# Performance work log

Measured on AMD Instinct MI355X. Metric: run time of the kernel, lower is better.

Reference implementation:

```python
import jax, jax.numpy as jnp
import numpy as np

D_ATTN = 64  # module's d_attn default; scale = rsqrt(64) regardless of real head dim


def setup_inputs() -> dict:
    key = jax.random.key(0)
    k0, k1, k2 = jax.random.split(key, 3)
    hidden = 256
    b, h, w = 8, 48, 48
    x = jax.random.normal(k0, (b, h, w, hidden * 2), dtype=jnp.float32)
    W1 = jax.random.normal(k1, (hidden * 2, hidden * 3), dtype=jnp.float32) * 0.02
    b1 = jnp.zeros((hidden * 3,), dtype=jnp.float32)
    W2 = jax.random.normal(k2, (hidden, hidden), dtype=jnp.float32) * 0.02
    b2 = jnp.zeros((hidden,), dtype=jnp.float32)
    return {"x": x, "W1": W1, "b1": b1, "W2": W2, "b2": b2}


def reference(x, W1, b1, W2, b2):
    b, h, w, c = x.shape
    n = h * w
    qkv = x @ W1 + b1                      # (b,h,w,3*hidden)
    q, k, v = jnp.split(qkv, 3, axis=-1)   # each (b,h,w,hidden)
    d = q.shape[-1]
    q = q.reshape(b, n, d)
    k = k.reshape(b, n, d)
    v = v.reshape(b, n, d)
    scale = 1.0 / jnp.sqrt(jnp.float32(D_ATTN))
    scores = jnp.einsum('bnd,bmd->bnm', q, k) * scale   # (b,n,n)
    attn = jax.nn.softmax(scores, axis=-1)
    out = jnp.einsum('bnm,bmd->bnd', attn, v)            # (b,n,d)
    out = out @ W2 + b2
    return out.reshape(b, h, w, d)
```

## Files before the change

kernel.cpp:

```cpp
#include <hip/hip_runtime.h>
#include <math.h>

typedef _Float16 f16;
typedef __attribute__((ext_vector_type(8))) _Float16 f16x8;
typedef __attribute__((ext_vector_type(4))) _Float16 f16x4;
typedef __attribute__((ext_vector_type(4))) float f32x4;

#define BB   8
#define NN   2304
#define CIN  512
#define HID  256
#define QKV3 768
#define MM   (BB * NN)
#define SCALE 0.125f

#define MFMA16(a, b, c) __builtin_amdgcn_mfma_f32_16x16x32_f16(a, b, c, 0, 0, 0)

__global__ __launch_bounds__(256) void transpose_f32_to_f16(
    const float* __restrict__ W, f16* __restrict__ Wt, int K, int N)
{
    __shared__ float tile[32][33];
    const int tx = threadIdx.x & 31, ty = threadIdx.x >> 5;
    const int n0 = blockIdx.x * 32, k0 = blockIdx.y * 32;
#pragma unroll
    for (int i = 0; i < 4; ++i)
        tile[ty + i * 8][tx] = W[(long)(k0 + ty + i * 8) * N + n0 + tx];
    __syncthreads();
#pragma unroll
    for (int i = 0; i < 4; ++i)
        Wt[(long)(n0 + ty + i * 8) * K + k0 + tx] = (f16)tile[tx][ty + i * 8];
}

template <int VAR>
__global__ __launch_bounds__(256) void gemm_mfma(
    const void* __restrict__ Ap, const f16* __restrict__ Bt,
    const float* __restrict__ bias, void* __restrict__ Cp,
    int Kdim, int Ndim, int NB)
{
    __shared__ char lds[32768];
    char* As = lds;
    char* Bs = lds + 16384;

    const int t = threadIdx.x;
    const int lane = t & 63;
    const int w = t >> 6;
    const int chunk = gridDim.x >> 3;
    const int bsw = (blockIdx.x & 7) * chunk + (blockIdx.x >> 3);
    const int m0 = (bsw / NB) * 128;
    const int n0 = (bsw % NB) * 128;
    const int wm = (w >> 1) * 64;
    const int wn = (w & 1) * 64;
    const int NK = Kdim >> 6;

    f32x4 acc[4][4];
#pragma unroll
    for (int i = 0; i < 4; ++i)
#pragma unroll
        for (int j = 0; j < 4; ++j) acc[i][j] = (f32x4){0.f, 0.f, 0.f, 0.f};

    float4 a32[8];
    int4   a16[4];
    int4   breg[4];

    auto loadA = [&](int kt) {
        if (VAR == 0) {
            const float* A = (const float*)Ap;
#pragma unroll
            for (int i = 0; i < 8; ++i) {
                const int cid = t + i * 256, row = cid >> 4, cir = cid & 15;
                a32[i] = *(const float4*)&A[(long)(m0 + row) * Kdim + kt * 64 + cir * 4];
            }
        } else {
            const f16* A = (const f16*)Ap;
#pragma unroll
            for (int i = 0; i < 4; ++i) {
                const int cid = t + i * 256, row = cid >> 3, cir = cid & 7;
                a16[i] = *(const int4*)&A[(long)(m0 + row) * Kdim + kt * 64 + cir * 8];
            }
        }
#pragma unroll
        for (int i = 0; i < 4; ++i) {
            const int cid = t + i * 256, row = cid >> 3, cir = cid & 7;
            breg[i] = *(const int4*)&Bt[(long)(n0 + row) * Kdim + kt * 64 + cir * 8];
        }
    };
    auto writeLDS = [&]() {
        if (VAR == 0) {
#pragma unroll
            for (int i = 0; i < 8; ++i) {
                const int cid = t + i * 256, row = cid >> 4, cir = cid & 15;
                f16x4 v = {(f16)a32[i].x, (f16)a32[i].y, (f16)a32[i].z, (f16)a32[i].w};
                *(f16x4*)(As + row * 128 + ((cir * 8) ^ ((row & 7) << 4))) = v;
            }
        } else {
#pragma unroll
            for (int i = 0; i < 4; ++i) {
                const int cid = t + i * 256, row = cid >> 3, cir = cid & 7;
                *(int4*)(As + row * 128 + ((cir * 16) ^ ((row & 7) << 4))) = a16[i];
            }
        }
#pragma unroll
        for (int i = 0; i < 4; ++i) {
            const int cid = t + i * 256, row = cid >> 3, cir = cid & 7;
            *(int4*)(Bs + row * 128 + ((cir * 16) ^ ((row & 7) << 4))) = breg[i];
        }
    };

    loadA(0);
    writeLDS();
    __syncthreads();

    for (int kt = 0; kt < NK; ++kt) {
        if (kt + 1 < NK) loadA(kt + 1);
#pragma unroll
        for (int ks = 0; ks < 2; ++ks) {
            f16x8 af[4], bf[4];
            const int kb = (ks * 32 + ((lane >> 4) * 8)) * 2;
#pragma unroll
            for (int mb = 0; mb < 4; ++mb) {
                const int row = wm + mb * 16 + (lane & 15);
                af[mb] = *(const f16x8*)(As + row * 128 + (kb ^ ((row & 7) << 4)));
            }
#pragma unroll
            for (int nb = 0; nb < 4; ++nb) {
                const int row = wn + nb * 16 + (lane & 15);
                bf[nb] = *(const f16x8*)(Bs + row * 128 + (kb ^ ((row & 7) << 4)));
            }
#pragma unroll
            for (int mb = 0; mb < 4; ++mb)
#pragma unroll
                for (int nb = 0; nb < 4; ++nb)
                    acc[mb][nb] = MFMA16(af[mb], bf[nb], acc[mb][nb]);
        }
        __syncthreads();
        if (kt + 1 < NK) { writeLDS(); __syncthreads(); }
    }

#pragma unroll
    for (int nb = 0; nb < 4; ++nb) {
        const int col = n0 + wn + nb * 16 + (lane & 15);
        const float bv = bias[col];
        const float sc = (VAR == 0 && col < HID) ? SCALE : 1.0f;
#pragma unroll
        for (int mb = 0; mb < 4; ++mb)
#pragma unroll
            for (int j = 0; j < 4; ++j) {
                const int row = m0 + wm + mb * 16 + (lane >> 4) * 4 + j;
                const float v = (acc[mb][nb][j] + bv) * sc;
                if (VAR == 0) ((f16*)Cp)[(long)row * Ndim + col] = (f16)v;
                else          ((float*)Cp)[(long)row * Ndim + col] = v;
            }
    }
}

#define QM 64
#define KT 64

__global__ __launch_bounds__(256) void attn_mfma(
    const f16* __restrict__ qkv, f16* __restrict__ attno)
{
    __shared__ char lds[73728];
    char* Ks = lds;
    char* Vt = lds + 32768;
    char* Pw = lds + 65536;

    const int t = threadIdx.x;
    const int lane = t & 63;
    const int w = t >> 6;
    const int b = blockIdx.x & 7;
    const int q0 = (blockIdx.x >> 3) * QM;
    const long base = (long)b * NN;

    const int qrow = q0 + w * 16 + (lane & 15);
    f16x8 qf[8];
    {
        const f16* qsrc = qkv + (base + qrow) * QKV3 + ((lane >> 4) * 8);
#pragma unroll
        for (int ks = 0; ks < 8; ++ks)
            qf[ks] = *(const f16x8*)(qsrc + ks * 32);
    }

    f32x4 o[16];
#pragma unroll
    for (int i = 0; i < 16; ++i) o[i] = (f32x4){0.f, 0.f, 0.f, 0.f};
    float m[4], lsum[4];
#pragma unroll
    for (int j = 0; j < 4; ++j) { m[j] = -1e30f; lsum[j] = 0.f; }

    const int vdg = (t >> 4) * 16;
    const int vquad = t & 15;

    for (int kt0 = 0; kt0 < NN; kt0 += KT) {
        int4 kreg[8];
#pragma unroll
        for (int i = 0; i < 8; ++i) {
            const int cid = t + i * 256, row = cid >> 5, cir = cid & 31;
            kreg[i] = *(const int4*)(qkv + (base + kt0 + row) * QKV3 + 256 + cir * 8);
        }
        __syncthreads();
#pragma unroll
        for (int i = 0; i < 8; ++i) {
            const int cid = t + i * 256, row = cid >> 5, cir = cid & 31;
            *(int4*)(Ks + row * 512 + ((cir * 16) ^ ((row & 15) << 4))) = kreg[i];
        }
        f16x8 vreg[8];
#pragma unroll
        for (int r = 0; r < 4; ++r) {
            const f16* vs = qkv + (base + kt0 + vquad * 4 + r) * QKV3 + 512 + vdg;
            vreg[r * 2]     = *(const f16x8*)(vs);
            vreg[r * 2 + 1] = *(const f16x8*)(vs + 8);
        }
#pragma unroll
        for (int i = 0; i < 16; ++i) {
            const int d = vdg + i;
            f16x4 wv;
#pragma unroll
            for (int r = 0; r < 4; ++r)
                wv[r] = (i < 8) ? vreg[r * 2][i] : vreg[r * 2 + 1][i - 8];
            *(f16x4*)(Vt + d * 128 + ((vquad * 8) ^ ((d & 7) << 4))) = wv;
        }
        __syncthreads();

        f32x4 s[4];
#pragma unroll
        for (int nb = 0; nb < 4; ++nb) s[nb] = (f32x4){0.f, 0.f, 0.f, 0.f};
#pragma unroll
        for (int ks = 0; ks < 8; ++ks) {
            const int kb = (ks * 32 + (lane >> 4) * 8) * 2;
#pragma unroll
            for (int nb = 0; nb < 4; ++nb) {
                const int row = nb * 16 + (lane & 15);
                f16x8 kf = *(const f16x8*)(Ks + row * 512 + (kb ^ ((row & 15) << 4)));
                s[nb] = MFMA16(qf[ks], kf, s[nb]);
            }
        }

        float f[4];
#pragma unroll
        for (int j = 0; j < 4; ++j) {
            float rmax = fmaxf(fmaxf(s[0][j], s[1][j]), fmaxf(s[2][j], s[3][j]));
            rmax = fmaxf(rmax, __shfl_xor(rmax, 1));
            rmax = fmaxf(rmax, __shfl_xor(rmax, 2));
            rmax = fmaxf(rmax, __shfl_xor(rmax, 4));
            rmax = fmaxf(rmax, __shfl_xor(rmax, 8));
            const float mnew = fmaxf(m[j], rmax);
            f[j] = __expf(m[j] - mnew);
            const float p0 = __expf(s[0][j] - mnew);
            const float p1 = __expf(s[1][j] - mnew);
            const float p2 = __expf(s[2][j] - mnew);
            const float p3 = __expf(s[3][j] - mnew);
            float ps = (p0 + p1) + (p2 + p3);
            ps += __shfl_xor(ps, 1);
            ps += __shfl_xor(ps, 2);
            ps += __shfl_xor(ps, 4);
            ps += __shfl_xor(ps, 8);
            lsum[j] = lsum[j] * f[j] + ps;
            m[j] = mnew;
            const int prow = (lane >> 4) * 4 + j;
            char* pr = Pw + w * 2048 + prow * 128;
            const int cb = (lane & 15) * 2;
            const int sw = (prow & 7) << 4;
            *(f16*)(pr + ((cb +  0) ^ sw)) = (f16)p0;
            *(f16*)(pr + ((cb + 32) ^ sw)) = (f16)p1;
            *(f16*)(pr + ((cb + 64) ^ sw)) = (f16)p2;
            *(f16*)(pr + ((cb + 96) ^ sw)) = (f16)p3;
        }
#pragma unroll
        for (int nb2 = 0; nb2 < 16; ++nb2)
#pragma unroll
            for (int j = 0; j < 4; ++j) o[nb2][j] *= f[j];

        asm volatile("s_waitcnt lgkmcnt(0)" ::: "memory");
        __builtin_amdgcn_sched_barrier(0);

#pragma unroll
        for (int ks2 = 0; ks2 < 2; ++ks2) {
            const int prow = lane & 15;
            const int kb = (ks2 * 32 + (lane >> 4) * 8) * 2;
            f16x8 pa = *(const f16x8*)(Pw + w * 2048 + prow * 128 + (kb ^ ((prow & 7) << 4)));
#pragma unroll
            for (int nb2 = 0; nb2 < 16; ++nb2) {
                const int d = nb2 * 16 + (lane & 15);
                f16x8 vb = *(const f16x8*)(Vt + d * 128 + (kb ^ ((d & 7) << 4)));
                o[nb2] = MFMA16(pa, vb, o[nb2]);
            }
        }
    }

    float rinv[4];
#pragma unroll
    for (int j = 0; j < 4; ++j) rinv[j] = 1.f / lsum[j];
#pragma unroll
    for (int nb2 = 0; nb2 < 16; ++nb2) {
        const int col = nb2 * 16 + (lane & 15);
#pragma unroll
        for (int j = 0; j < 4; ++j) {
            const int row = q0 + w * 16 + (lane >> 4) * 4 + j;
            attno[(base + row) * HID + col] = (f16)(o[nb2][j] * rinv[j]);
        }
    }
}

extern "C" void kernel_launch(void* const* d_in, const int* in_sizes, int n_in,
                              void* d_out, int out_size, void* d_ws, size_t ws_size,
                              hipStream_t stream)
{
    (void)in_sizes; (void)n_in; (void)out_size; (void)ws_size;
    const float* x  = (const float*)d_in[0];
    const float* W1 = (const float*)d_in[1];
    const float* b1 = (const float*)d_in[2];
    const float* W2 = (const float*)d_in[3];
    const float* b2 = (const float*)d_in[4];
    float* out = (float*)d_out;

    char* ws = (char*)d_ws;
    f16* W1t   = (f16*)ws;
    f16* W2t   = (f16*)(ws + 786432);
    f16* qkv   = (f16*)(ws + 786432 + 131072);
    f16* attno = (f16*)(ws + 786432 + 131072 + 28311552);

    transpose_f32_to_f16<<<dim3(QKV3 / 32, CIN / 32), 256, 0, stream>>>(W1, W1t, CIN, QKV3);
    transpose_f32_to_f16<<<dim3(HID / 32, HID / 32), 256, 0, stream>>>(W2, W2t, HID, HID);
    gemm_mfma<0><<<864, 256, 0, stream>>>(x, W1t, b1, qkv, CIN, QKV3, 6);
    attn_mfma<<<288, 256, 0, stream>>>(qkv, attno);
    gemm_mfma<1><<<288, 256, 0, stream>>>(attno, W2t, b2, out, HID, HID, 2);
}
```

Baseline: 555.3 us.

## Split attention KV range across wave pairs with register prefetch and merge

```diff
diff --git a/kernel.cpp b/kernel.cpp
--- a/kernel.cpp
+++ b/kernel.cpp
@@ -153,25 +153,32 @@
     }
 }
 
-#define QM 64
-#define KT 64
-
-__global__ __launch_bounds__(256) void attn_mfma(
+#define QM 32
+#define KT 32
+#define KVHALF 1152
+#define NT (KVHALF / KT)
+
+__global__ __launch_bounds__(256, 2) void attn_mfma(
     const f16* __restrict__ qkv, f16* __restrict__ attno)
 {
-    __shared__ char lds[73728];
-    char* Ks = lds;
-    char* Vt = lds + 32768;
-    char* Pw = lds + 65536;
-
-    const int t = threadIdx.x;
+    __shared__ char lds[69888];
+
+    const int t    = threadIdx.x;
     const int lane = t & 63;
-    const int w = t >> 6;
-    const int b = blockIdx.x & 7;
-    const int q0 = (blockIdx.x >> 3) * QM;
+    const int w    = t >> 6;
+    const int rg   = w & 1;
+    const int kh   = w >> 1;
+    const int tt   = t & 127;
+    const int b    = blockIdx.x & 7;
+    const int q0   = (blockIdx.x >> 3) * QM;
     const long base = (long)b * NN;
-
-    const int qrow = q0 + w * 16 + (lane & 15);
+    const int kv0  = kh * KVHALF;
+
+    char* KsH = lds + kh * 16384;
+    char* VtH = lds + 32768 + kh * 16384;
+    char* PwW = lds + 65536 + w * 1024;
+
+    const int qrow = q0 + rg * 16 + (lane & 15);
     f16x8 qf[8];
     {
         const f16* qsrc = qkv + (base + qrow) * QKV3 + ((lane >> 4) * 8);
@@ -187,28 +194,30 @@
 #pragma unroll
     for (int j = 0; j < 4; ++j) { m[j] = -1e30f; lsum[j] = 0.f; }
 
-    const int vdg = (t >> 4) * 16;
-    const int vquad = t & 15;
-
-    for (int kt0 = 0; kt0 < NN; kt0 += KT) {
-        int4 kreg[8];
+    const int vquad = tt & 7;
+    const int vdg   = (tt >> 3) * 16;
+
+    int4  kreg[8];
+    f16x8 vreg[8];
+    auto loadTile = [&](int tile) {
+        const long kbase = base + kv0 + tile * KT;
 #pragma unroll
         for (int i = 0; i < 8; ++i) {
-            const int cid = t + i * 256, row = cid >> 5, cir = cid & 31;
-            kreg[i] = *(const int4*)(qkv + (base + kt0 + row) * QKV3 + 256 + cir * 8);
-        }
-        __syncthreads();
-#pragma unroll
-        for (int i = 0; i < 8; ++i) {
-            const int cid = t + i * 256, row = cid >> 5, cir = cid & 31;
-            *(int4*)(Ks + row * 512 + ((cir * 16) ^ ((row & 15) << 4))) = kreg[i];
-        }
-        f16x8 vreg[8];
+            const int cid = tt + i * 128, row = cid >> 5, cir = cid & 31;
+            kreg[i] = *(const int4*)(qkv + (kbase + row) * QKV3 + 256 + cir * 8);
+        }
 #pragma unroll
         for (int r = 0; r < 4; ++r) {
-            const f16* vs = qkv + (base + kt0 + vquad * 4 + r) * QKV3 + 512 + vdg;
+            const f16* vs = qkv + (kbase + vquad * 4 + r) * QKV3 + 512 + vdg;
             vreg[r * 2]     = *(const f16x8*)(vs);
             vreg[r * 2 + 1] = *(const f16x8*)(vs + 8);
+        }
+    };
+    auto writeTile = [&]() {
+#pragma unroll
+        for (int i = 0; i < 8; ++i) {
+            const int cid = tt + i * 128, row = cid >> 5, cir = cid & 31;
+            *(int4*)(KsH + row * 512 + ((cir * 16) ^ ((row & 15) << 4))) = kreg[i];
         }
 #pragma unroll
         for (int i = 0; i < 16; ++i) {
@@ -217,28 +226,38 @@
 #pragma unroll
             for (int r = 0; r < 4; ++r)
                 wv[r] = (i < 8) ? vreg[r * 2][i] : vreg[r * 2 + 1][i - 8];
-            *(f16x4*)(Vt + d * 128 + ((vquad * 8) ^ ((d & 7) << 4))) = wv;
-        }
+            *(f16x4*)(VtH + d * 64 + ((vquad * 8) ^ ((d & 3) << 4))) = wv;
+        }
+    };
+
+    loadTile(0);
+
+    for (int tile = 0; tile < NT; ++tile) {
         __syncthreads();
-
-        f32x4 s[4];
-#pragma unroll
-        for (int nb = 0; nb < 4; ++nb) s[nb] = (f32x4){0.f, 0.f, 0.f, 0.f};
+        writeTile();
+        __syncthreads();
+        if (tile + 1 < NT) loadTile(tile + 1);
+
+        f32x4 s[2];
+        s[0] = (f32x4){0.f, 0.f, 0.f, 0.f};
+        s[1] = (f32x4){0.f, 0.f, 0.f, 0.f};
+        __builtin_amdgcn_s_setprio(1);
 #pragma unroll
         for (int ks = 0; ks < 8; ++ks) {
             const int kb = (ks * 32 + (lane >> 4) * 8) * 2;
 #pragma unroll
-            for (int nb = 0; nb < 4; ++nb) {
+            for (int nb = 0; nb < 2; ++nb) {
                 const int row = nb * 16 + (lane & 15);
-                f16x8 kf = *(const f16x8*)(Ks + row * 512 + (kb ^ ((row & 15) << 4)));
+                f16x8 kf = *(const f16x8*)(KsH + row * 512 + (kb ^ ((row & 15) << 4)));
                 s[nb] = MFMA16(qf[ks], kf, s[nb]);
             }
         }
+        __builtin_amdgcn_s_setprio(0);
 
         float f[4];
 #pragma unroll
         for (int j = 0; j < 4; ++j) {
-            float rmax = fmaxf(fmaxf(s[0][j], s[1][j]), fmaxf(s[2][j], s[3][j]));
+            float rmax = fmaxf(s[0][j], s[1][j]);
             rmax = fmaxf(rmax, __shfl_xor(rmax, 1));
             rmax = fmaxf(rmax, __shfl_xor(rmax, 2));
             rmax = fmaxf(rmax, __shfl_xor(rmax, 4));
@@ -247,9 +266,7 @@
             f[j] = __expf(m[j] - mnew);
             const float p0 = __expf(s[0][j] - mnew);
             const float p1 = __expf(s[1][j] - mnew);
-            const float p2 = __expf(s[2][j] - mnew);
-            const float p3 = __expf(s[3][j] - mnew);
-            float ps = (p0 + p1) + (p2 + p3);
+            float ps = p0 + p1;
             ps += __shfl_xor(ps, 1);
             ps += __shfl_xor(ps, 2);
             ps += __shfl_xor(ps, 4);
@@ -257,13 +274,11 @@
             lsum[j] = lsum[j] * f[j] + ps;
             m[j] = mnew;
             const int prow = (lane >> 4) * 4 + j;
-            char* pr = Pw + w * 2048 + prow * 128;
+            char* pr = PwW + prow * 64;
             const int cb = (lane & 15) * 2;
-            const int sw = (prow & 7) << 4;
+            const int sw = (prow & 3) << 4;
             *(f16*)(pr + ((cb +  0) ^ sw)) = (f16)p0;
             *(f16*)(pr + ((cb + 32) ^ sw)) = (f16)p1;
-            *(f16*)(pr + ((cb + 64) ^ sw)) = (f16)p2;
-            *(f16*)(pr + ((cb + 96) ^ sw)) = (f16)p3;
         }
 #pragma unroll
         for (int nb2 = 0; nb2 < 16; ++nb2)
@@ -273,30 +288,58 @@
         asm volatile("s_waitcnt lgkmcnt(0)" ::: "memory");
         __builtin_amdgcn_sched_barrier(0);
 
-#pragma unroll
-        for (int ks2 = 0; ks2 < 2; ++ks2) {
+        {
             const int prow = lane & 15;
-            const int kb = (ks2 * 32 + (lane >> 4) * 8) * 2;
-            f16x8 pa = *(const f16x8*)(Pw + w * 2048 + prow * 128 + (kb ^ ((prow & 7) << 4)));
+            const int kb = (lane >> 4) * 16;
+            f16x8 pa = *(const f16x8*)(PwW + prow * 64 + (kb ^ ((prow & 3) << 4)));
+            __builtin_amdgcn_s_setprio(1);
 #pragma unroll
             for (int nb2 = 0; nb2 < 16; ++nb2) {
                 const int d = nb2 * 16 + (lane & 15);
-                f16x8 vb = *(const f16x8*)(Vt + d * 128 + (kb ^ ((d & 7) << 4)));
+                f16x8 vb = *(const f16x8*)(VtH + d * 64 + (kb ^ ((d & 3) << 4)));
                 o[nb2] = MFMA16(pa, vb, o[nb2]);
             }
-        }
-    }
-
-    float rinv[4];
-#pragma unroll
-    for (int j = 0; j < 4; ++j) rinv[j] = 1.f / lsum[j];
-#pragma unroll
-    for (int nb2 = 0; nb2 < 16; ++nb2) {
-        const int col = nb2 * 16 + (lane & 15);
+            __builtin_amdgcn_s_setprio(0);
+        }
+    }
+
+    __syncthreads();
+    if (kh == 1) {
+        float* oL = (float*)(lds + rg * 16384);
+#pragma unroll
+        for (int nb2 = 0; nb2 < 16; ++nb2)
+#pragma unroll
+            for (int j = 0; j < 4; ++j)
+                oL[((lane >> 4) * 4 + j) * 256 + nb2 * 16 + (lane & 15)] = o[nb2][j];
+        if ((lane & 15) == 0) {
+            float* ml = (float*)(lds + 69632 + rg * 128);
+#pragma unroll
+            for (int j = 0; j < 4; ++j) {
+                const int row = (lane >> 4) * 4 + j;
+                ml[row * 2]     = m[j];
+                ml[row * 2 + 1] = lsum[j];
+            }
+        }
+    }
+    __syncthreads();
+    if (kh == 0) {
+        const float* oL = (const float*)(lds + rg * 16384);
+        const float* ml = (const float*)(lds + 69632 + rg * 128);
 #pragma unroll
         for (int j = 0; j < 4; ++j) {
-            const int row = q0 + w * 16 + (lane >> 4) * 4 + j;
-            attno[(base + row) * HID + col] = (f16)(o[nb2][j] * rinv[j]);
+            const int row = (lane >> 4) * 4 + j;
+            const float m1 = ml[row * 2];
+            const float l1 = ml[row * 2 + 1];
+            const float M  = fmaxf(m[j], m1);
+            const float e0 = __expf(m[j] - M);
+            const float e1 = __expf(m1 - M);
+            const float inv = 1.f / (lsum[j] * e0 + l1 * e1);
+#pragma unroll
+            for (int nb2 = 0; nb2 < 16; ++nb2) {
+                const int col = nb2 * 16 + (lane & 15);
+                const float v = (o[nb2][j] * e0 + oL[row * 256 + col] * e1) * inv;
+                attno[(base + q0 + rg * 16 + row) * HID + col] = (f16)v;
+            }
         }
     }
 }
@@ -322,6 +365,6 @@
     transpose_f32_to_f16<<<dim3(QKV3 / 32, CIN / 32), 256, 0, stream>>>(W1, W1t, CIN, QKV3);
     transpose_f32_to_f16<<<dim3(HID / 32, HID / 32), 256, 0, stream>>>(W2, W2t, HID, HID);
     gemm_mfma<0><<<864, 256, 0, stream>>>(x, W1t, b1, qkv, CIN, QKV3, 6);
-    attn_mfma<<<288, 256, 0, stream>>>(qkv, attno);
+    attn_mfma<<<576, 256, 0, stream>>>(qkv, attno);
     gemm_mfma<1><<<288, 256, 0, stream>>>(attno, W2t, b2, out, HID, HID, 2);
 }
```

New measurement: 513.8 us. -7.5%, faster.
